# Kernel tuning notes

Hardware: AMD Instinct MI355X
Metric: run time of the kernel (lower is better)

Reference implementation:

```python
import jax, jax.numpy as jnp
import numpy as np

T, D_MODEL = 2048, 6144
NH, NKV, HD = 48, 8, 128
THETA, CAP = 10000.0, 30.0


def setup_inputs() -> dict:
    key = jax.random.key(0)
    k1, k2, k3 = jax.random.split(key, 3)
    return {
        "positions": jnp.arange(T, dtype=jnp.int32),
        "hidden_states": jax.random.normal(k1, (T, D_MODEL), jnp.float32),
        "w_qkv": jax.random.normal(k2, (D_MODEL, (NH + 2 * NKV) * HD), jnp.float32) * 0.02,
        "w_o": jax.random.normal(k3, (NH * HD, D_MODEL), jnp.float32) * 0.02,
    }


def _rope_neox(positions, x):
    # x: [T, h, HD]; neox-style: rotate concatenated halves
    half = HD // 2
    inv_freq = 1.0 / (THETA ** (jnp.arange(0, HD, 2, dtype=jnp.float32) / HD))  # [half]
    freqs = positions.astype(jnp.float32)[:, None] * inv_freq  # [T, half]
    cos = jnp.cos(freqs)[:, None, :]  # [T,1,half]
    sin = jnp.sin(freqs)[:, None, :]
    x1, x2 = x[..., :half], x[..., half:]
    return jnp.concatenate([x1 * cos - x2 * sin, x2 * cos + x1 * sin], axis=-1)


def reference(positions, hidden_states, w_qkv, w_o):
    qkv = hidden_states @ w_qkv  # [T, (NH+2*NKV)*HD]
    q, k, v = jnp.split(qkv, [NH * HD, NH * HD + NKV * HD], axis=-1)
    q = q.reshape(T, NH, HD)
    k = k.reshape(T, NKV, HD)
    v = v.reshape(T, NKV, HD)
    q = _rope_neox(positions, q)
    k = _rope_neox(positions, k)
    # GQA: expand kv heads to query heads
    g = NH // NKV
    k = jnp.repeat(k, g, axis=1)  # [T, NH, HD]
    v = jnp.repeat(v, g, axis=1)
    scale = HD ** -0.5
    logits = jnp.einsum('thd,shd->hts', q, k) * scale  # [NH, T, T]
    logits = CAP * jnp.tanh(logits / CAP)  # tanh logit softcapping
    causal = positions[:, None] >= positions[None, :]  # [T, T]
    logits = jnp.where(causal[None, :, :], logits, -jnp.inf)
    probs = jax.nn.softmax(logits, axis=-1)
    out = jnp.einsum('hts,shd->thd', probs, v)  # [T, NH, HD]
    out = out.reshape(T, NH * HD)
    return out @ w_o
```

## Files before the change

kernel.cpp:

```cpp
#include <hip/hip_runtime.h>
#include <hip/hip_bf16.h>
#include <stdint.h>

#define TSEQ   2048
#define DMODEL 6144
#define NHEADS 48
#define NKVH   8
#define HDIM   128
#define QKVC   8192
#define GRP    6

typedef __attribute__((ext_vector_type(8))) short short8;
typedef __attribute__((ext_vector_type(4))) float f32x4;


__device__ __forceinline__ unsigned short f2b(float f) {
  union { float f; unsigned int u; } v; v.f = f;
  unsigned int u = v.u;
  unsigned int r = (u + 0x7FFFu + ((u >> 16) & 1u)) >> 16;
  return (unsigned short)r;
}

#if __has_builtin(__builtin_amdgcn_exp2f)
#define EXP2(x) __builtin_amdgcn_exp2f(x)
#else
#define EXP2(x) exp2f(x)
#endif
#if __has_builtin(__builtin_amdgcn_rcpf)
#define RCP(x) __builtin_amdgcn_rcpf(x)
#else
#define RCP(x) (1.0f / (x))
#endif

typedef const __attribute__((address_space(1))) void* as1_cvp;
typedef __attribute__((address_space(3))) void* as3_vp;

__device__ __forceinline__ void gload_lds16(const void* g, void* l) {
  __builtin_amdgcn_global_load_lds(
      (as1_cvp)(uintptr_t)g,
      (as3_vp)(unsigned int)(uintptr_t)l, 16, 0, 0);
}

#define LGKMC(n) do { asm volatile("s_waitcnt lgkmcnt(" #n ")" ::: "memory"); \
                      __builtin_amdgcn_sched_barrier(0); } while (0)
#define VMC(n) do { asm volatile("s_waitcnt vmcnt(" #n ")" ::: "memory"); \
                    __builtin_amdgcn_sched_barrier(0); } while (0)
#define BARR  do { asm volatile("s_barrier" ::: "memory"); } while (0)


__global__ __launch_bounds__(256) void k_cvt(const float* __restrict__ in,
                                             unsigned short* __restrict__ outp, int n) {
  int i = (blockIdx.x * 256 + threadIdx.x) * 8;
  if (i + 7 < n) {
    float4 va = *(const float4*)(in + i);
    float4 vb = *(const float4*)(in + i + 4);
    union { unsigned short s[8]; uint4 u; } o;
    o.s[0] = f2b(va.x); o.s[1] = f2b(va.y); o.s[2] = f2b(va.z); o.s[3] = f2b(va.w);
    o.s[4] = f2b(vb.x); o.s[5] = f2b(vb.y); o.s[6] = f2b(vb.z); o.s[7] = f2b(vb.w);
    *(uint4*)(outp + i) = o.u;
  }
}

__global__ __launch_bounds__(256) void k_tr2(const float* __restrict__ in, long istr, long zin,
                                             unsigned short* __restrict__ out, long ostr, long zout) {
  __shared__ unsigned short tile[64][68];
  const int tid = threadIdx.x;
  const int br = blockIdx.y * 64;
  const int bc = blockIdx.x * 64;
  in  += (size_t)blockIdx.z * zin;
  out += (size_t)blockIdx.z * zout;
  const int row = tid >> 4;
  const int c4  = (tid & 15) * 4;
#pragma unroll
  for (int p = 0; p < 4; ++p) {
    const int r = p * 16 + row;
    float4 v = *(const float4*)(in + (size_t)(br + r) * istr + bc + c4);
    tile[r][c4 + 0] = f2b(v.x);
    tile[r][c4 + 1] = f2b(v.y);
    tile[r][c4 + 2] = f2b(v.z);
    tile[r][c4 + 3] = f2b(v.w);
  }
  __syncthreads();
#pragma unroll
  for (int p = 0; p < 4; ++p) {
    const int r = p * 16 + row;
    union { unsigned short s[4]; uint2 u; } o;
    o.s[0] = tile[c4 + 0][r];
    o.s[1] = tile[c4 + 1][r];
    o.s[2] = tile[c4 + 2][r];
    o.s[3] = tile[c4 + 3][r];
    *(uint2*)(out + (size_t)(bc + r) * ostr + br + c4) = o.u;
  }
}

__global__ void k_trig(const int* __restrict__ pos, float* __restrict__ cs,
                       float* __restrict__ sn) {
  int t = blockIdx.x, i = threadIdx.x;
  float p = (float)pos[t];
  float inv = EXP2(-(float)(2 * i) * (1.0f / 128.0f) * 13.287712379549449f);
  float f = p * inv;
  cs[t * 64 + i] = cosf(f);
  sn[t * 64 + i] = sinf(f);
}


#define READ_A(mh, aa) do { \
  _Pragma("unroll") for (int m = 0; m < 4; ++m) \
  _Pragma("unroll") for (int ks = 0; ks < 2; ++ks) \
    aa[m][ks] = *(const short8*)(LA + (wm * 128 + (mh) * 64 + m * 16 + lr) * 128 \
                                 + ((ks * 64 + lkb) ^ lsw)); } while (0)

#define READ_B(nh, bb) do { \
  _Pragma("unroll") for (int n2 = 0; n2 < 2; ++n2) \
  _Pragma("unroll") for (int ks = 0; ks < 2; ++ks) \
    bb[n2][ks] = *(const short8*)(LB + (wn * 64 + (nh) * 32 + n2 * 16 + lr) * 128 \
                                  + ((ks * 64 + lkb) ^ lsw)); } while (0)

#define CLUSTER(mh, nh, aa, bb) do { \
  __builtin_amdgcn_s_setprio(1); \
  _Pragma("unroll") for (int m = 0; m < 4; ++m) \
  _Pragma("unroll") for (int n2 = 0; n2 < 2; ++n2) \
  _Pragma("unroll") for (int ks = 0; ks < 2; ++ks) \
    acc[(mh) * 4 + m][(nh) * 2 + n2] = __builtin_amdgcn_mfma_f32_16x16x32_bf16( \
        aa[m][ks], bb[n2][ks], acc[(mh) * 4 + m][(nh) * 2 + n2], 0, 0, 0); \
  __builtin_amdgcn_s_setprio(0); } while (0)

#define STAGE_A(kt, bb) do { \
  _Pragma("unroll") for (int i = 0; i < 4; ++i) \
    gload_lds16(Asrc + (size_t)(kt) * 64 + (size_t)i * 64 * K, \
                lds + (bb) * 65536 + F + i * 8192); } while (0)

#define STAGE_B(kt, bb) do { \
  _Pragma("unroll") for (int i = 0; i < 4; ++i) \
    gload_lds16(Bsrc + (size_t)(kt) * 64 + (size_t)i * 64 * K, \
                lds + (bb) * 65536 + 32768 + F + i * 8192); } while (0)

__global__ __launch_bounds__(512, 2) void k_gemm8(const unsigned short* __restrict__ A,
                                                  const unsigned short* __restrict__ Bt,
                                                  float* __restrict__ C,
                                                  int M, int N, int K) {
  extern __shared__ __align__(16) unsigned char lds[];
  const int tid  = threadIdx.x;
  const int lane = tid & 63;
  const int wave = tid >> 6;
  const int wm = wave >> 2;
  const int wn = wave & 3;
  const int lr  = lane & 15;
  const int lkb = (lane >> 4) * 16;
  const int li4 = (lane >> 4) * 4;
  const int lsw = (lane & 7) << 4;

  const int mt = M >> 8;
  const int nt = N >> 8;
  const int Cx = nt >> 3;
  const int lin = blockIdx.x;
  const int xcd = lin & 7;
  const int r   = lin >> 3;
  const int m0  = (r % mt) << 8;
  const int n0  = (xcd * Cx + r / mt) << 8;

  const int F   = tid * 16;
  const int r0  = F >> 7;
  const int cbs = (F & 127) ^ ((r0 & 7) << 4);
  const unsigned short* Asrc = A  + (size_t)(m0 + r0) * K + (cbs >> 1);
  const unsigned short* Bsrc = Bt + (size_t)(n0 + r0) * K + (cbs >> 1);

  const int NT = K >> 6;

  f32x4 acc[8][4];
#pragma unroll
  for (int i = 0; i < 8; ++i)
#pragma unroll
    for (int j = 0; j < 4; ++j) acc[i][j] = (f32x4){0.f, 0.f, 0.f, 0.f};

  STAGE_A(0, 0);
  STAGE_B(0, 0);
  STAGE_A(1, 1);
  VMC(4);
  BARR;

  for (int t = 0; t < NT; ++t) {
    const int cur = t & 1;
    const unsigned char* LA = lds + cur * 65536;
    const unsigned char* LB = LA + 32768;
    short8 a0[4][2], a1[4][2], b0[2][2], b1[2][2];

    READ_A(0, a0);
    READ_B(0, b0);
    if (t + 1 < NT) STAGE_B(t + 1, cur ^ 1);
    READ_B(1, b1);
    READ_A(1, a1);

    LGKMC(12);
    CLUSTER(0, 0, a0, b0);
    LGKMC(8);
    CLUSTER(0, 1, a0, b1);
    LGKMC(0);
    CLUSTER(1, 0, a1, b0);
    BARR;
    if (t + 2 < NT) STAGE_A(t + 2, cur);
    CLUSTER(1, 1, a1, b1);
    if (t + 2 < NT) { VMC(4); } else { VMC(0); }
    BARR;
  }

#pragma unroll
  for (int mh = 0; mh < 2; ++mh)
#pragma unroll
    for (int m = 0; m < 4; ++m)
#pragma unroll
      for (int nh = 0; nh < 2; ++nh)
#pragma unroll
        for (int n2 = 0; n2 < 2; ++n2)
#pragma unroll
          for (int i = 0; i < 4; ++i) {
            int row = m0 + wm * 128 + mh * 64 + m * 16 + li4 + i;
            int col = n0 + wn * 64 + nh * 32 + n2 * 16 + lr;
            C[(size_t)row * N + col] = acc[mh * 4 + m][nh * 2 + n2][i];
          }
}


__global__ __launch_bounds__(256) void k_rope(const float* __restrict__ qkv,
                                              const float* __restrict__ cs,
                                              const float* __restrict__ sn,
                                              unsigned short* __restrict__ Q,
                                              unsigned short* __restrict__ K) {
  const int t = blockIdx.x;
  const int tid = threadIdx.x;
  const float* row = qkv + (size_t)t * QKVC;
  const float* c = cs + t * 64;
  const float* s = sn + t * 64;
  for (int p = tid; p < 56 * 16; p += 256) {
    const int h = p >> 4, q4 = (p & 15) * 4;
    const float* src = row + h * 128;
    float4 x1 = *(const float4*)(src + q4);
    float4 x2 = *(const float4*)(src + 64 + q4);
    float4 cc = *(const float4*)(c + q4);
    float4 ss = *(const float4*)(s + q4);
    unsigned short* dst = (h < NHEADS)
        ? Q + ((size_t)h * TSEQ + t) * HDIM
        : K + ((size_t)(h - NHEADS) * TSEQ + t) * HDIM;
    union { unsigned short sh[4]; uint2 u; } o1, o2;
    o1.sh[0] = f2b(x1.x * cc.x - x2.x * ss.x);
    o1.sh[1] = f2b(x1.y * cc.y - x2.y * ss.y);
    o1.sh[2] = f2b(x1.z * cc.z - x2.z * ss.z);
    o1.sh[3] = f2b(x1.w * cc.w - x2.w * ss.w);
    o2.sh[0] = f2b(x2.x * cc.x + x1.x * ss.x);
    o2.sh[1] = f2b(x2.y * cc.y + x1.y * ss.y);
    o2.sh[2] = f2b(x2.z * cc.z + x1.z * ss.z);
    o2.sh[3] = f2b(x2.w * cc.w + x1.w * ss.w);
    *(uint2*)(dst + q4) = o1.u;
    *(uint2*)(dst + 64 + q4) = o2.u;
  }
}


__global__ __launch_bounds__(256, 3) void k_attn2(const unsigned short* __restrict__ Q,
                                                  const unsigned short* __restrict__ K,
                                                  const unsigned short* __restrict__ V,
                                                  unsigned short* __restrict__ O) {
  __shared__ __align__(16) unsigned char KsB[16384];
  __shared__ __align__(16) unsigned char VsB[16384];
  __shared__ __align__(16) unsigned char PsB[4][2048];

  const int lin = blockIdx.x;
  const int g   = lin & 7;
  const int rr  = lin >> 3;
  const int hg  = rr % 6;
  const int pr  = rr / 6;
  const int h   = g * 6 + hg;
  const int tid = threadIdx.x, wave = tid >> 6, lane = tid & 63;
  const int lr = lane & 15, lk = (lane >> 4) * 8, li4 = (lane >> 4) * 4;
  const unsigned short* Qh = Q + (size_t)h * (TSEQ * HDIM);
  const unsigned char*  Kb = (const unsigned char*)(K + (size_t)g * (TSEQ * HDIM));
  const unsigned char*  Vb = (const unsigned char*)(V + (size_t)g * (TSEQ * HDIM));
  unsigned char* Pw = PsB[wave];

  for (int half = 0; half < 2; ++half) {
    const int j  = half ? (31 - pr) : pr;
    const int t0 = j * 64 + wave * 16;
    const int nst = j + 1;

    short8 qf[4];
#pragma unroll
    for (int ks = 0; ks < 4; ++ks)
      qf[ks] = *(const short8*)(Qh + (size_t)(t0 + lr) * HDIM + ks * 32 + lk);

    f32x4 oacc[8];
#pragma unroll
    for (int n = 0; n < 8; ++n) oacc[n] = (f32x4){0.f, 0.f, 0.f, 0.f};
    float rs4[4] = {0.f, 0.f, 0.f, 0.f};

    for (int st = 0; st < nst; ++st) {
      const int s0 = st * 64;
#pragma unroll
      for (int c = 0; c < 4; ++c) {
        const int FF = tid * 16 + c * 4096;
        const int krow = FF >> 8;
        const int kcol = (FF & 255) ^ ((krow & 7) << 4);
        gload_lds16(Kb + (size_t)(s0 + krow) * 256 + kcol, KsB + FF);
        const int vrow = FF >> 7;
        const int vcol = (FF & 127) ^ ((vrow & 7) << 4);
        gload_lds16(Vb + (size_t)vrow * (TSEQ * 2) + (size_t)s0 * 2 + vcol, VsB + FF);
      }
      __syncthreads();

      f32x4 sacc[4];
#pragma unroll
      for (int n = 0; n < 4; ++n) sacc[n] = (f32x4){0.f, 0.f, 0.f, 0.f};
#pragma unroll
      for (int ks = 0; ks < 4; ++ks) {
        short8 kf[4];
#pragma unroll
        for (int n = 0; n < 4; ++n) {
          const int row = n * 16 + lr;
          kf[n] = *(const short8*)(KsB + row * 256 + ((ks * 64 + lk * 2) ^ ((row & 7) << 4)));
        }
#pragma unroll
        for (int n = 0; n < 4; ++n)
          sacc[n] = __builtin_amdgcn_mfma_f32_16x16x32_bf16(qf[ks], kf[n], sacc[n], 0, 0, 0);
      }

      const bool lastst = (st == nst - 1);
#pragma unroll
      for (int n = 0; n < 4; ++n)
#pragma unroll
        for (int i = 0; i < 4; ++i) {
          float sv = sacc[n][i] * 0.08838834764831845f;
          float e = EXP2(sv * 0.09617966939259757f);
          float p = EXP2(-86.5617024533378f * RCP(e + 1.0f));
          if (lastst && (s0 + n * 16 + lr > t0 + li4 + i)) p = 0.f;
          rs4[i] += p;
          const int prow = li4 + i;
          *(unsigned short*)(Pw + prow * 128 +
              (((n * 16 + lr) * 2) ^ ((prow & 7) << 4))) = f2b(p);
        }

#pragma unroll
      for (int ks2 = 0; ks2 < 2; ++ks2) {
        short8 pf = *(const short8*)(Pw + lr * 128 +
                         (((ks2 * 32 + lk) * 2) ^ ((lr & 7) << 4)));
        short8 vf[8];
#pragma unroll
        for (int n = 0; n < 8; ++n) {
          const int row = n * 16 + lr;
          vf[n] = *(const short8*)(VsB + row * 128 + ((ks2 * 64 + lk * 2) ^ ((row & 7) << 4)));
        }
#pragma unroll
        for (int n = 0; n < 8; ++n)
          oacc[n] = __builtin_amdgcn_mfma_f32_16x16x32_bf16(pf, vf[n], oacc[n], 0, 0, 0);
      }
      __syncthreads();
    }

    float inv4[4];
#pragma unroll
    for (int i = 0; i < 4; ++i) {
      float v = rs4[i];
      v += __shfl_xor(v, 1, 64);
      v += __shfl_xor(v, 2, 64);
      v += __shfl_xor(v, 4, 64);
      v += __shfl_xor(v, 8, 64);
      inv4[i] = RCP(v);
    }
#pragma unroll
    for (int n = 0; n < 8; ++n)
#pragma unroll
      for (int i = 0; i < 4; ++i)
        O[(size_t)(t0 + li4 + i) * DMODEL + h * HDIM + n * 16 + lr] =
            f2b(oacc[n][i] * inv4[i]);
  }
}


extern "C" void kernel_launch(void* const* d_in, const int* in_sizes, int n_in,
                              void* d_out, int out_size, void* d_ws, size_t ws_size,
                              hipStream_t stream) {
  const int*   pos  = (const int*)d_in[0];
  const float* hid  = (const float*)d_in[1];
  const float* wqkv = (const float*)d_in[2];
  const float* wo   = (const float*)d_in[3];
  float* out = (float*)d_out;
  char* ws = (char*)d_ws;

  const size_t O_XB   = 0;
  const size_t O_WQT  = 25165824;
  const size_t O_WOT  = 125829120;
  const size_t O_QKV  = 201326592;
  const size_t O_TRIG = 268435456;

  unsigned short* Xb  = (unsigned short*)(ws + O_XB);
  unsigned short* Wqt = (unsigned short*)(ws + O_WQT);
  unsigned short* Wot = (unsigned short*)(ws + O_WOT);
  float* QKV = (float*)(ws + O_QKV);
  float* CS  = (float*)(ws + O_TRIG);
  float* SN  = CS + TSEQ * 64;
  unsigned short* Qr = Wqt;
  unsigned short* Kr = Wqt + (size_t)NHEADS * TSEQ * HDIM;
  unsigned short* Vt = Kr + (size_t)NKVH * TSEQ * HDIM;
  unsigned short* AO = Xb;

  hipFuncSetAttribute((const void*)k_gemm8,
                      hipFuncAttributeMaxDynamicSharedMemorySize, 131072);

  k_cvt<<<(TSEQ * DMODEL) / (256 * 8), 256, 0, stream>>>(hid, Xb, TSEQ * DMODEL);
  k_tr2<<<dim3(QKVC / 64, DMODEL / 64, 1), 256, 0, stream>>>(wqkv, QKVC, 0, Wqt, DMODEL, 0);
  k_tr2<<<dim3(DMODEL / 64, DMODEL / 64, 1), 256, 0, stream>>>(wo, DMODEL, 0, Wot, DMODEL, 0);
  k_trig<<<TSEQ, 64, 0, stream>>>(pos, CS, SN);

  k_gemm8<<<(TSEQ / 256) * (QKVC / 256), 512, 131072, stream>>>(Xb, Wqt, QKV,
                                                                TSEQ, QKVC, DMODEL);
  k_rope<<<TSEQ, 256, 0, stream>>>(QKV, CS, SN, Qr, Kr);
  k_tr2<<<dim3(HDIM / 64, TSEQ / 64, NKVH), 256, 0, stream>>>(
      QKV + (size_t)(DMODEL + NKVH * HDIM), QKVC, HDIM,
      Vt, TSEQ, (size_t)HDIM * TSEQ);
  k_attn2<<<768, 256, 0, stream>>>(Qr, Kr, Vt, AO);
  k_gemm8<<<(TSEQ / 256) * (DMODEL / 256), 512, 131072, stream>>>(AO, Wot, out,
                                                                  TSEQ, DMODEL, DMODEL);
}
```

Baseline: 552.2 us.

## Restructure GEMM pipeline into quarter-tile stages with interleaved wave mapping

Changes the wave-to-subtile mapping so each 128-row/col half of the LDS tile is read by all waves together, and splits global-to-LDS staging into half-tile pieces issued between the four MFMA clusters. The prefetch depth drops from staging A two tiles ahead to one tile ahead, and barriers are added after each cluster so freed LDS halves can be refilled early. The aim is finer-grained overlap of loads with MFMA. The cost is many more barriers per k-step and a shallower prefetch, which may expose memory latency.

Measured after the change: 578.0 us. 4.7% more time.

```diff
diff --git a/kernel.cpp b/kernel.cpp
--- a/kernel.cpp
+++ b/kernel.cpp
@@ -107,13 +107,13 @@
 #define READ_A(mh, aa) do { \
   _Pragma("unroll") for (int m = 0; m < 4; ++m) \
   _Pragma("unroll") for (int ks = 0; ks < 2; ++ks) \
-    aa[m][ks] = *(const short8*)(LA + (wm * 128 + (mh) * 64 + m * 16 + lr) * 128 \
+    aa[m][ks] = *(const short8*)(LA + ((mh) * 128 + wm * 64 + m * 16 + lr) * 128 \
                                  + ((ks * 64 + lkb) ^ lsw)); } while (0)
 
 #define READ_B(nh, bb) do { \
   _Pragma("unroll") for (int n2 = 0; n2 < 2; ++n2) \
   _Pragma("unroll") for (int ks = 0; ks < 2; ++ks) \
-    bb[n2][ks] = *(const short8*)(LB + (wn * 64 + (nh) * 32 + n2 * 16 + lr) * 128 \
+    bb[n2][ks] = *(const short8*)(LB + ((nh) * 128 + wn * 32 + n2 * 16 + lr) * 128 \
                                   + ((ks * 64 + lkb) ^ lsw)); } while (0)
 
 #define CLUSTER(mh, nh, aa, bb) do { \
@@ -125,13 +125,13 @@
         aa[m][ks], bb[n2][ks], acc[(mh) * 4 + m][(nh) * 2 + n2], 0, 0, 0); \
   __builtin_amdgcn_s_setprio(0); } while (0)
 
-#define STAGE_A(kt, bb) do { \
-  _Pragma("unroll") for (int i = 0; i < 4; ++i) \
+#define STAGE_AH(kt, bb, hf) do { \
+  _Pragma("unroll") for (int i = (hf) * 2; i < (hf) * 2 + 2; ++i) \
     gload_lds16(Asrc + (size_t)(kt) * 64 + (size_t)i * 64 * K, \
                 lds + (bb) * 65536 + F + i * 8192); } while (0)
 
-#define STAGE_B(kt, bb) do { \
-  _Pragma("unroll") for (int i = 0; i < 4; ++i) \
+#define STAGE_BH(kt, bb, hf) do { \
+  _Pragma("unroll") for (int i = (hf) * 2; i < (hf) * 2 + 2; ++i) \
     gload_lds16(Bsrc + (size_t)(kt) * 64 + (size_t)i * 64 * K, \
                 lds + (bb) * 65536 + 32768 + F + i * 8192); } while (0)
 
@@ -173,34 +173,51 @@
 #pragma unroll
     for (int j = 0; j < 4; ++j) acc[i][j] = (f32x4){0.f, 0.f, 0.f, 0.f};
 
-  STAGE_A(0, 0);
-  STAGE_B(0, 0);
-  STAGE_A(1, 1);
-  VMC(4);
+  STAGE_AH(0, 0, 0);
+  STAGE_BH(0, 0, 0);
+  STAGE_BH(0, 0, 1);
+  STAGE_AH(0, 0, 1);
+  VMC(0);
   BARR;
 
   for (int t = 0; t < NT; ++t) {
     const int cur = t & 1;
+    const int nxt = cur ^ 1;
     const unsigned char* LA = lds + cur * 65536;
     const unsigned char* LB = LA + 32768;
     short8 a0[4][2], a1[4][2], b0[2][2], b1[2][2];
+    const bool more = (t + 1 < NT);
 
     READ_A(0, a0);
     READ_B(0, b0);
-    if (t + 1 < NT) STAGE_B(t + 1, cur ^ 1);
+    if (more) STAGE_AH(t + 1, nxt, 0);
+    LGKMC(8);
+    BARR;
+    LGKMC(0);
+    CLUSTER(0, 0, a0, b0);
+    if (more) { VMC(4); } else { VMC(2); }
+    BARR;
+
     READ_B(1, b1);
+    if (more) STAGE_BH(t + 1, nxt, 0);
+    BARR;
+    LGKMC(0);
+    CLUSTER(0, 1, a0, b1);
+    if (more) { VMC(4); } else { VMC(0); }
+    BARR;
+
     READ_A(1, a1);
-
-    LGKMC(12);
-    CLUSTER(0, 0, a0, b0);
-    LGKMC(8);
-    CLUSTER(0, 1, a0, b1);
+    if (more) STAGE_BH(t + 1, nxt, 1);
+    BARR;
     LGKMC(0);
     CLUSTER(1, 0, a1, b0);
     BARR;
-    if (t + 2 < NT) STAGE_A(t + 2, cur);
+
+    if (more) STAGE_AH(t + 1, nxt, 1);
+    BARR;
+    LGKMC(0);
     CLUSTER(1, 1, a1, b1);
-    if (t + 2 < NT) { VMC(4); } else { VMC(0); }
+    VMC(4);
     BARR;
   }
 
@@ -214,8 +231,8 @@
         for (int n2 = 0; n2 < 2; ++n2)
 #pragma unroll
           for (int i = 0; i < 4; ++i) {
-            int row = m0 + wm * 128 + mh * 64 + m * 16 + li4 + i;
-            int col = n0 + wn * 64 + nh * 32 + n2 * 16 + lr;
+            int row = m0 + mh * 128 + wm * 64 + m * 16 + li4 + i;
+            int col = n0 + nh * 128 + wn * 32 + n2 * 16 + lr;
             C[(size_t)row * N + col] = acc[mh * 4 + m][nh * 2 + n2][i];
           }
 }
```
